# Optimization experiments

Hardware: AMD Instinct MI355X
Metric: run time of the kernel (lower is better)

Reference implementation:

```python
import jax, jax.numpy as jnp
import numpy as np

NQ = 5          # qubits
DIM = 2 ** NQ   # 32 amplitudes
NL = 4          # StronglyEntanglingLayers depth


def _rot_matrix(phi, theta, omega):
    """PennyLane Rot(phi,theta,omega) = RZ(omega) @ RY(theta) @ RZ(phi)."""
    c = jnp.cos(theta / 2)
    s = jnp.sin(theta / 2)
    ep = jnp.exp(-0.5j * (phi + omega).astype(jnp.complex64))
    em = jnp.exp(-0.5j * (phi - omega).astype(jnp.complex64))
    return jnp.array([[0, 0], [0, 0]], jnp.complex64).at[0, 0].set(ep * c).at[0, 1].set(-jnp.conj(em) * s).at[1, 0].set(em * s).at[1, 1].set(jnp.conj(ep) * c)


def _apply_1q(state, U, w):
    # state: (B, 2,2,2,2,2); apply 2x2 U on qubit axis w
    state = jnp.moveaxis(state, w + 1, -1)
    state = state @ U.T
    return jnp.moveaxis(state, -1, w + 1)


def _apply_cnot(state, c, t):
    # flip target axis on the control=1 slice
    s0 = jax.lax.index_in_dim(state, 0, axis=c + 1, keepdims=True)
    s1 = jax.lax.index_in_dim(state, 1, axis=c + 1, keepdims=True)
    s1 = jnp.flip(s1, axis=t + 1)
    return jnp.concatenate([s0, s1], axis=c + 1)


def setup_inputs() -> dict:
    key = jax.random.key(0)
    k1, k2 = jax.random.split(key)
    inputs = jax.random.normal(k1, (524288, 30), dtype=jnp.float32)
    weights = jax.random.normal(k2, (NL, NQ, 3), dtype=jnp.float32)
    return {"inputs": inputs, "weights": weights}


def reference(inputs, weights):
    B = inputs.shape[0]
    # AmplitudeEmbedding: pad with zeros to 32 amplitudes, normalize per sample
    padded = jnp.pad(inputs, ((0, 0), (0, DIM - inputs.shape[1])))
    norm = jnp.linalg.norm(padded, axis=1, keepdims=True)
    state = (padded / norm).astype(jnp.complex64)
    state = state.reshape((B,) + (2,) * NQ)

    # StronglyEntanglingLayers
    for l in range(NL):
        for w in range(NQ):
            U = _rot_matrix(weights[l, w, 0], weights[l, w, 1], weights[l, w, 2])
            state = _apply_1q(state, U, w)
        r = (l % (NQ - 1)) + 1  # default imprimitive range pattern
        for w in range(NQ):
            state = _apply_cnot(state, w, (w + r) % NQ)

    # expval(PauliZ(i)) for each wire
    probs = jnp.abs(state) ** 2  # (B,2,2,2,2,2)
    evs = []
    for w in range(NQ):
        axes = tuple(a for a in range(1, NQ + 1) if a != w + 1)
        p = probs.sum(axis=axes)  # (B,2)
        evs.append(p[:, 0] - p[:, 1])
    return jnp.stack(evs, axis=1)  # (B, NQ)
```

## Files before the change

kernel.cpp:

```cpp
#include <hip/hip_runtime.h>

#define NQ 5
#define DIM 32
#define NL 4
#define NFEAT 30
#define NGATES (NL * NQ)

typedef float f32x4 __attribute__((ext_vector_type(4)));
typedef float f32x2 __attribute__((ext_vector_type(2)));
typedef short bf16x8 __attribute__((ext_vector_type(8)));

static __device__ __forceinline__ unsigned short f2bf(float f) {
    unsigned u = __float_as_uint(f);
    u += 0x7FFFu + ((u >> 16) & 1u);
    return (unsigned short)(u >> 16);
}

static __device__ __forceinline__ unsigned cvt_pk_bf16(float a, float b) {
    unsigned d;
    asm("v_cvt_pk_bf16_f32 %0, %1, %2" : "=v"(d) : "v"(a), "v"(b));
    return d;
}

__global__ __launch_bounds__(128) void build_unitary(const float* __restrict__ W,
                                                     unsigned short* __restrict__ Ubf) {
    __shared__ __align__(16) float g[NGATES][8];

    const int t = threadIdx.x;
    if (t < NGATES) {
        const float phi = W[t * 3 + 0];
        const float th  = W[t * 3 + 1];
        const float om  = W[t * 3 + 2];
        const float c = cosf(0.5f * th), s = sinf(0.5f * th);
        const float a  = 0.5f * (phi + om);
        const float bb = 0.5f * (phi - om);
        const float epr = cosf(a),  epi = -sinf(a);
        const float emr = cosf(bb), emi = -sinf(bb);
        g[t][0] = epr * c;   g[t][1] = epi * c;
        g[t][2] = -emr * s;  g[t][3] = emi * s;
        g[t][4] = emr * s;   g[t][5] = emi * s;
        g[t][6] = epr * c;   g[t][7] = -epi * c;
    }
    __syncthreads();

    const int z = t & 31;
    const int j = blockIdx.x * 4 + (t >> 5);

    float ar = (z == j) ? 1.0f : 0.0f;
    float ai = 0.0f;

#pragma unroll
    for (int l = 0; l < NL; ++l) {
#pragma unroll
        for (int w = 0; w < NQ; ++w) {
            const int gi = l * NQ + w;
            const f32x4 glo = *reinterpret_cast<const f32x4*>(&g[gi][0]);
            const f32x4 ghi = *reinterpret_cast<const f32x4*>(&g[gi][4]);
            const int shift = 4 - w;
            const int msk = 1 << shift;
            const int bit = (z >> shift) & 1;
            const float pr = __shfl_xor(ar, msk, 32);
            const float pi = __shfl_xor(ai, msk, 32);
            const float csr = bit ? ghi.z : glo.x;
            const float csi = bit ? ghi.w : glo.y;
            const float cpr = bit ? ghi.x : glo.z;
            const float cpi = bit ? ghi.y : glo.w;
            const float nar = csr * ar - csi * ai + cpr * pr - cpi * pi;
            const float nai = csr * ai + csi * ar + cpr * pi + cpi * pr;
            ar = nar; ai = nai;
        }
        const int r = (l % (NQ - 1)) + 1;
#pragma unroll
        for (int cq = 0; cq < NQ; ++cq) {
            const int tq = (cq + r) % NQ;
            const int cs = 4 - cq, ts = 4 - tq;
            const int tmask = 1 << ts;
            const float pr = __shfl_xor(ar, tmask, 32);
            const float pi = __shfl_xor(ai, tmask, 32);
            const int ctrl = (z >> cs) & 1;
            ar = ctrl ? pr : ar;
            ai = ctrl ? pi : ai;
        }
    }

    Ubf[(2 * z + 0) * 32 + j] = f2bf(ar);
    Ubf[(2 * z + 1) * 32 + j] = f2bf(ai);
}

__global__ __launch_bounds__(256) void qforward(const float* __restrict__ X,
                                                const unsigned short* __restrict__ Ubf,
                                                float* __restrict__ out, int B) {
    __shared__ __align__(16) float xs[4 * 64 * NFEAT];
    const int tid  = threadIdx.x;
    const int b0   = blockIdx.x * 256;
    const int lane = tid & 63;
    const int g    = lane >> 4;
    const int r    = lane & 15;
    const int wv   = tid >> 6;

    bf16x8 afrag[4];
#pragma unroll
    for (int t = 0; t < 4; ++t)
        afrag[t] = *reinterpret_cast<const bf16x8*>(Ubf + (16 * t + r) * 32 + g * 8);

    const long Btot  = (long)B * NFEAT;
    const long gbase = (long)b0 * NFEAT + wv * (64 * NFEAT);
    float* lbase = &xs[wv * (64 * NFEAT)];
#pragma unroll
    for (int it = 0; it < 8; ++it) {
        const int fi = it * 256 + lane * 4;
        if (fi < 64 * NFEAT && gbase + fi + 4 <= Btot)
            __builtin_amdgcn_global_load_lds(
                (const __attribute__((address_space(1))) unsigned*)(X + gbase + fi),
                (__attribute__((address_space(3))) unsigned*)(lbase + fi),
                16, 0, 2 );
    }
    asm volatile("s_waitcnt vmcnt(0)" ::: "memory");

    const float sg2 = (g & 2) ? -1.f : 1.f;
    const float sg3 = (g & 1) ? -1.f : 1.f;

#pragma unroll
    for (int st = 0; st < 4; ++st) {
        const float* rowp = lbase + (st * 16 + r) * NFEAT + g * 8;

        f32x2 v0 = *reinterpret_cast<const f32x2*>(rowp + 0);
        f32x2 v1 = *reinterpret_cast<const f32x2*>(rowp + 2);
        f32x2 v2 = *reinterpret_cast<const f32x2*>(rowp + 4);
        f32x2 v3 = (g == 3) ? (f32x2){0.f, 0.f}
                            : *reinterpret_cast<const f32x2*>(rowp + 6);

        bf16x8 bfrag;
        unsigned* bw = reinterpret_cast<unsigned*>(&bfrag);
        bw[0] = cvt_pk_bf16(v0.x, v0.y);
        bw[1] = cvt_pk_bf16(v1.x, v1.y);
        bw[2] = cvt_pk_bf16(v2.x, v2.y);
        bw[3] = cvt_pk_bf16(v3.x, v3.y);

        f32x4 d[4];
#pragma unroll
        for (int t = 0; t < 4; ++t)
            d[t] = __builtin_amdgcn_mfma_f32_16x16x32_bf16(
                afrag[t], bfrag, (f32x4){0.f, 0.f, 0.f, 0.f}, 0, 0, 0);

        float ev0 = 0.f, ev1 = 0.f, ev2 = 0.f, ev3 = 0.f, ev4 = 0.f, nrm = 0.f;
#pragma unroll
        for (int t = 0; t < 4; ++t) {
            const float p0 = d[t].x * d[t].x + d[t].y * d[t].y;
            const float p1 = d[t].z * d[t].z + d[t].w * d[t].w;
            const float pt = p0 + p1;
            nrm += pt;
            ev0 += (t & 2) ? -pt : pt;
            ev1 += (t & 1) ? -pt : pt;
            ev2 = fmaf(sg2, pt, ev2);
            ev3 = fmaf(sg3, pt, ev3);
            ev4 += p0 - p1;
        }
        ev0 += __shfl_xor(ev0, 16, 64); ev0 += __shfl_xor(ev0, 32, 64);
        ev1 += __shfl_xor(ev1, 16, 64); ev1 += __shfl_xor(ev1, 32, 64);
        ev2 += __shfl_xor(ev2, 16, 64); ev2 += __shfl_xor(ev2, 32, 64);
        ev3 += __shfl_xor(ev3, 16, 64); ev3 += __shfl_xor(ev3, 32, 64);
        ev4 += __shfl_xor(ev4, 16, 64); ev4 += __shfl_xor(ev4, 32, 64);
        nrm += __shfl_xor(nrm, 16, 64); nrm += __shfl_xor(nrm, 32, 64);

        if (g == 0) {
            const int s = b0 + wv * 64 + st * 16 + r;
            if (s < B) {
                const float inv = 1.0f / nrm;
                __builtin_nontemporal_store(ev0 * inv, &out[s * NQ + 0]);
                __builtin_nontemporal_store(ev1 * inv, &out[s * NQ + 1]);
                __builtin_nontemporal_store(ev2 * inv, &out[s * NQ + 2]);
                __builtin_nontemporal_store(ev3 * inv, &out[s * NQ + 3]);
                __builtin_nontemporal_store(ev4 * inv, &out[s * NQ + 4]);
            }
        }
    }
}

extern "C" void kernel_launch(void* const* d_in, const int* in_sizes, int n_in,
                              void* d_out, int out_size, void* d_ws, size_t ws_size,
                              hipStream_t stream) {
    const float* X = (const float*)d_in[0];
    const float* W = (const float*)d_in[1];
    float* out = (float*)d_out;
    const int B = in_sizes[0] / NFEAT;

    unsigned short* Ubf = (unsigned short*)d_ws;

    build_unitary<<<8, 128, 0, stream>>>(W, Ubf);

    const int nblocks = (B + 255) / 256;
    qforward<<<nblocks, 256, 0, stream>>>(X, Ubf, out, B);
}
```

Baseline: 22.14 us.

## Process four tiles per block with double-buffered LDS prefetch

Each block now handles four 256-sample tiles instead of one, using two LDS buffers so the global-to-LDS load of the next tile overlaps compute on the current one. Output stores are deferred to the end and spread across the four lane groups, so each group writes one expectation value instead of group 0 writing all five. This amortizes the unitary-fragment load and block launch overhead over more work, and cuts the grid to a quarter. In exchange LDS doubles to about 60KB per block, which may limit occupancy, and the vmcnt(8) waits depend on the exact count of loads issued per stage.

Result: slower. 23.62 us (+6.7%).

```diff
diff --git a/kernel.cpp b/kernel.cpp
--- a/kernel.cpp
+++ b/kernel.cpp
@@ -90,88 +90,122 @@
 __global__ __launch_bounds__(256) void qforward(const float* __restrict__ X,
                                                 const unsigned short* __restrict__ Ubf,
                                                 float* __restrict__ out, int B) {
-    __shared__ __align__(16) float xs[4 * 64 * NFEAT];
+    __shared__ __align__(16) float xs[2][4 * 64 * NFEAT];
     const int tid  = threadIdx.x;
-    const int b0   = blockIdx.x * 256;
     const int lane = tid & 63;
     const int g    = lane >> 4;
     const int r    = lane & 15;
     const int wv   = tid >> 6;
 
+    const int ntiles = (B + 255) >> 8;
+    const int t0 = blockIdx.x * 4;
+
     bf16x8 afrag[4];
 #pragma unroll
     for (int t = 0; t < 4; ++t)
         afrag[t] = *reinterpret_cast<const bf16x8*>(Ubf + (16 * t + r) * 32 + g * 8);
 
-    const long Btot  = (long)B * NFEAT;
-    const long gbase = (long)b0 * NFEAT + wv * (64 * NFEAT);
-    float* lbase = &xs[wv * (64 * NFEAT)];
-#pragma unroll
-    for (int it = 0; it < 8; ++it) {
-        const int fi = it * 256 + lane * 4;
-        if (fi < 64 * NFEAT && gbase + fi + 4 <= Btot)
-            __builtin_amdgcn_global_load_lds(
-                (const __attribute__((address_space(1))) unsigned*)(X + gbase + fi),
-                (__attribute__((address_space(3))) unsigned*)(lbase + fi),
-                16, 0, 2 );
-    }
-    asm volatile("s_waitcnt vmcnt(0)" ::: "memory");
+    const long Btot = (long)B * NFEAT;
+
+    auto stage = [&](int tile, int buf) {
+        if (tile >= ntiles) return;
+        const long gbase = (long)tile * (256 * NFEAT) + wv * (64 * NFEAT);
+        float* lb = &xs[buf][wv * (64 * NFEAT)];
+#pragma unroll
+        for (int it = 0; it < 8; ++it) {
+            const int fi = it * 256 + lane * 4;
+            if (fi < 64 * NFEAT && gbase + fi + 4 <= Btot)
+                __builtin_amdgcn_global_load_lds(
+                    (const __attribute__((address_space(1))) unsigned*)(X + gbase + fi),
+                    (__attribute__((address_space(3))) unsigned*)(lb + fi),
+                    16, 0, 2 );
+        }
+    };
 
     const float sg2 = (g & 2) ? -1.f : 1.f;
     const float sg3 = (g & 1) ? -1.f : 1.f;
 
-#pragma unroll
-    for (int st = 0; st < 4; ++st) {
-        const float* rowp = lbase + (st * 16 + r) * NFEAT + g * 8;
-
-        f32x2 v0 = *reinterpret_cast<const f32x2*>(rowp + 0);
-        f32x2 v1 = *reinterpret_cast<const f32x2*>(rowp + 2);
-        f32x2 v2 = *reinterpret_cast<const f32x2*>(rowp + 4);
-        f32x2 v3 = (g == 3) ? (f32x2){0.f, 0.f}
-                            : *reinterpret_cast<const f32x2*>(rowp + 6);
-
-        bf16x8 bfrag;
-        unsigned* bw = reinterpret_cast<unsigned*>(&bfrag);
-        bw[0] = cvt_pk_bf16(v0.x, v0.y);
-        bw[1] = cvt_pk_bf16(v1.x, v1.y);
-        bw[2] = cvt_pk_bf16(v2.x, v2.y);
-        bw[3] = cvt_pk_bf16(v3.x, v3.y);
-
-        f32x4 d[4];
-#pragma unroll
-        for (int t = 0; t < 4; ++t)
-            d[t] = __builtin_amdgcn_mfma_f32_16x16x32_bf16(
-                afrag[t], bfrag, (f32x4){0.f, 0.f, 0.f, 0.f}, 0, 0, 0);
-
-        float ev0 = 0.f, ev1 = 0.f, ev2 = 0.f, ev3 = 0.f, ev4 = 0.f, nrm = 0.f;
-#pragma unroll
-        for (int t = 0; t < 4; ++t) {
-            const float p0 = d[t].x * d[t].x + d[t].y * d[t].y;
-            const float p1 = d[t].z * d[t].z + d[t].w * d[t].w;
-            const float pt = p0 + p1;
-            nrm += pt;
-            ev0 += (t & 2) ? -pt : pt;
-            ev1 += (t & 1) ? -pt : pt;
-            ev2 = fmaf(sg2, pt, ev2);
-            ev3 = fmaf(sg3, pt, ev3);
-            ev4 += p0 - p1;
-        }
-        ev0 += __shfl_xor(ev0, 16, 64); ev0 += __shfl_xor(ev0, 32, 64);
-        ev1 += __shfl_xor(ev1, 16, 64); ev1 += __shfl_xor(ev1, 32, 64);
-        ev2 += __shfl_xor(ev2, 16, 64); ev2 += __shfl_xor(ev2, 32, 64);
-        ev3 += __shfl_xor(ev3, 16, 64); ev3 += __shfl_xor(ev3, 32, 64);
-        ev4 += __shfl_xor(ev4, 16, 64); ev4 += __shfl_xor(ev4, 32, 64);
-        nrm += __shfl_xor(nrm, 16, 64); nrm += __shfl_xor(nrm, 32, 64);
-
-        if (g == 0) {
-            const int s = b0 + wv * 64 + st * 16 + r;
+    float oA[4][4], oB[4][4];
+
+#define COMPUTE_TILE(I)                                                          \
+    {                                                                            \
+        const float* lbase = &xs[(I) & 1][wv * (64 * NFEAT)];                    \
+        _Pragma("unroll")                                                        \
+        for (int st = 0; st < 4; ++st) {                                         \
+            const float* rowp = lbase + (st * 16 + r) * NFEAT + g * 8;           \
+            f32x2 v0 = *reinterpret_cast<const f32x2*>(rowp + 0);                \
+            f32x2 v1 = *reinterpret_cast<const f32x2*>(rowp + 2);                \
+            f32x2 v2 = *reinterpret_cast<const f32x2*>(rowp + 4);                \
+            f32x2 v3 = (g == 3) ? (f32x2){0.f, 0.f}                              \
+                                : *reinterpret_cast<const f32x2*>(rowp + 6);     \
+            bf16x8 bfrag;                                                        \
+            unsigned* bw = reinterpret_cast<unsigned*>(&bfrag);                  \
+            bw[0] = cvt_pk_bf16(v0.x, v0.y);                                     \
+            bw[1] = cvt_pk_bf16(v1.x, v1.y);                                     \
+            bw[2] = cvt_pk_bf16(v2.x, v2.y);                                     \
+            bw[3] = cvt_pk_bf16(v3.x, v3.y);                                     \
+            f32x4 d[4];                                                          \
+            _Pragma("unroll")                                                    \
+            for (int t = 0; t < 4; ++t)                                          \
+                d[t] = __builtin_amdgcn_mfma_f32_16x16x32_bf16(                  \
+                    afrag[t], bfrag, (f32x4){0.f, 0.f, 0.f, 0.f}, 0, 0, 0);      \
+            float ev0 = 0.f, ev1 = 0.f, ev2 = 0.f, ev3 = 0.f, ev4 = 0.f,         \
+                  nrm = 0.f;                                                     \
+            _Pragma("unroll")                                                    \
+            for (int t = 0; t < 4; ++t) {                                        \
+                const float p0 = d[t].x * d[t].x + d[t].y * d[t].y;              \
+                const float p1 = d[t].z * d[t].z + d[t].w * d[t].w;              \
+                const float pt = p0 + p1;                                        \
+                nrm += pt;                                                       \
+                ev0 += (t & 2) ? -pt : pt;                                       \
+                ev1 += (t & 1) ? -pt : pt;                                       \
+                ev2 = fmaf(sg2, pt, ev2);                                        \
+                ev3 = fmaf(sg3, pt, ev3);                                        \
+                ev4 += p0 - p1;                                                  \
+            }                                                                    \
+            ev0 += __shfl_xor(ev0, 16, 64); ev0 += __shfl_xor(ev0, 32, 64);      \
+            ev1 += __shfl_xor(ev1, 16, 64); ev1 += __shfl_xor(ev1, 32, 64);      \
+            ev2 += __shfl_xor(ev2, 16, 64); ev2 += __shfl_xor(ev2, 32, 64);      \
+            ev3 += __shfl_xor(ev3, 16, 64); ev3 += __shfl_xor(ev3, 32, 64);      \
+            ev4 += __shfl_xor(ev4, 16, 64); ev4 += __shfl_xor(ev4, 32, 64);      \
+            nrm += __shfl_xor(nrm, 16, 64); nrm += __shfl_xor(nrm, 32, 64);      \
+            const float inv = 1.0f / nrm;                                        \
+            const float mine = (g == 0) ? ev0 : (g == 1) ? ev1                   \
+                             : (g == 2) ? ev2 : ev3;                             \
+            oA[(I)][st] = mine * inv;                                            \
+            oB[(I)][st] = ev4 * inv;                                             \
+        }                                                                        \
+    }
+
+    stage(t0 + 0, 0);
+    stage(t0 + 1, 1);
+    asm volatile("s_waitcnt vmcnt(8)" ::: "memory");
+    __builtin_amdgcn_sched_barrier(0);
+    COMPUTE_TILE(0)
+    asm volatile("" ::: "memory");
+    stage(t0 + 2, 0);
+    asm volatile("s_waitcnt vmcnt(8)" ::: "memory");
+    __builtin_amdgcn_sched_barrier(0);
+    COMPUTE_TILE(1)
+    asm volatile("" ::: "memory");
+    stage(t0 + 3, 1);
+    asm volatile("s_waitcnt vmcnt(8)" ::: "memory");
+    __builtin_amdgcn_sched_barrier(0);
+    COMPUTE_TILE(2)
+    asm volatile("s_waitcnt vmcnt(0)" ::: "memory");
+    __builtin_amdgcn_sched_barrier(0);
+    COMPUTE_TILE(3)
+#undef COMPUTE_TILE
+
+#pragma unroll
+    for (int i = 0; i < 4; ++i) {
+#pragma unroll
+        for (int st = 0; st < 4; ++st) {
+            const int s = (t0 + i) * 256 + wv * 64 + st * 16 + r;
             if (s < B) {
-                const float inv = 1.0f / nrm;
-                __builtin_nontemporal_store(ev0 * inv, &out[s * NQ + 0]);
-                __builtin_nontemporal_store(ev1 * inv, &out[s * NQ + 1]);
-                __builtin_nontemporal_store(ev2 * inv, &out[s * NQ + 2]);
-                __builtin_nontemporal_store(ev3 * inv, &out[s * NQ + 3]);
-                __builtin_nontemporal_store(ev4 * inv, &out[s * NQ + 4]);
+                __builtin_nontemporal_store(oA[i][st], &out[s * NQ + g]);
+                if (g == 0)
+                    __builtin_nontemporal_store(oB[i][st], &out[s * NQ + 4]);
             }
         }
     }
@@ -189,6 +223,7 @@
 
     build_unitary<<<8, 128, 0, stream>>>(W, Ubf);
 
-    const int nblocks = (B + 255) / 256;
+    const int ntiles = (B + 255) / 256;
+    const int nblocks = (ntiles + 3) / 4;
     qforward<<<nblocks, 256, 0, stream>>>(X, Ubf, out, B);
 }
```
